# Performance work log

Hardware: AMD Instinct MI355X
Metric: run time of the kernel (lower is better)

## Reference

```python
import jax, jax.numpy as jnp
import numpy as np

B, S, E, H = 4, 4096, 1024, 16
D = E // H          # head dim 64
C = 128             # chunk_size
O = 32              # overlap_size
KCTX = C + O        # context length for chunks > 0
SCALE = 1.0 / np.sqrt(D)


def setup_inputs() -> dict:
    key = jax.random.key(0)
    ks = jax.random.split(key, 11)
    s = 1.0 / np.sqrt(E)
    f32 = jnp.float32
    return {
        "query": jax.random.normal(ks[0], (B, S, E), f32),
        "key_in": jax.random.normal(ks[1], (B, S, E), f32),
        "value": jax.random.normal(ks[2], (B, S, E), f32),
        "Wq": jax.random.normal(ks[3], (E, E), f32) * s,
        "bq": jnp.zeros((E,), f32),
        "Wk": jax.random.normal(ks[4], (E, E), f32) * s,
        "bk": jnp.zeros((E,), f32),
        "Wv": jax.random.normal(ks[5], (E, E), f32) * s,
        "bv": jnp.zeros((E,), f32),
        "Wo": jax.random.normal(ks[6], (E, E), f32) * s,
        "bo": jnp.zeros((E,), f32),
    }


def _attn(q, k, v):
    # q: [..., Lq, H, D], k/v: [..., Lk, H, D] -> [..., Lq, E]
    scores = jnp.einsum("...qhd,...khd->...hqk", q, k) * SCALE
    p = jax.nn.softmax(scores, axis=-1)
    o = jnp.einsum("...hqk,...khd->...qhd", p, v)
    return o.reshape(o.shape[:-2] + (E,))


def reference(query, key_in, value, Wq, bq, Wk, bk, Wv, bv, Wo, bo):
    # position-wise projections (done once; identical to per-chunk projection)
    q = (query @ Wq + bq).reshape(B, S, H, D)
    k = (key_in @ Wk + bk).reshape(B, S, H, D)
    v = (value @ Wv + bv).reshape(B, S, H, D)

    n = S // C  # number of chunks

    # chunk 0: self-attention over first C positions, all C outputs kept
    out0 = _attn(q[:, :C], k[:, :C], v[:, :C])  # [B, C, E]

    # chunks 1..n-1: torch code drops the first O query outputs of each chunk,
    # so only queries at positions i*C+O .. (i+1)*C-1 survive. Each softmax row
    # depends only on its own query, so compute just the kept rows.
    qr = q[:, C:].reshape(B, n - 1, C, H, D)[:, :, O:]  # [B, n-1, C-O, H, D]
    # overlapping kv context windows: [i*C - O, (i+1)*C) of length C+O
    idx = jnp.arange(1, n)[:, None] * C - O + jnp.arange(KCTX)[None, :]  # [n-1, KCTX]
    kr = k[:, idx]  # [B, n-1, KCTX, H, D]
    vr = v[:, idx]
    outr = _attn(qr, kr, vr)               # [B, n-1, C-O, E]
    outr = outr.reshape(B, (n - 1) * (C - O), E)

    out = jnp.concatenate([out0, outr], axis=1)  # [B, C + (n-1)*(C-O), E]
    return out @ Wo + bo
```

## Files before the change

kernel.cpp:

```cpp
#include <hip/hip_runtime.h>
#include <hip/hip_bf16.h>

typedef __bf16 bf16x8 __attribute__((ext_vector_type(8)));
typedef float f32x4 __attribute__((ext_vector_type(4)));
typedef unsigned short u16;
typedef unsigned int u32;

#define DEV __device__ __forceinline__
#define MFMA16 __builtin_amdgcn_mfma_f32_16x16x32_bf16

DEV u16 f2b(float f) {
  __hip_bfloat16 h = __float2bfloat16(f);
  return __builtin_bit_cast(u16, h);
}

DEV void gl_lds16(const u16* g, u16* l) {
  __builtin_amdgcn_global_load_lds(
      (const __attribute__((address_space(1))) void*)g,
      (__attribute__((address_space(3))) void*)l, 16, 0, 0);
}

__global__ __launch_bounds__(256) void wcvt_all(
    const float* __restrict__ Wq, const float* __restrict__ Wk,
    const float* __restrict__ Wv, const float* __restrict__ Wo,
    u16* __restrict__ WtQ, u16* __restrict__ WtK,
    u16* __restrict__ WtV, u16* __restrict__ WtO,
    const float* __restrict__ query, u16* __restrict__ qc,
    const float* __restrict__ key_in, u16* __restrict__ kc,
    const float* __restrict__ value, u16* __restrict__ vc) {
  __shared__ u16 ls[64 * 80];
  const int t = threadIdx.x;
  const int bid = blockIdx.x;
  if (bid < 1024) {
    const int wsel = bid >> 8;
    const float* W = (wsel == 0) ? Wq : (wsel == 1) ? Wk : (wsel == 2) ? Wv : Wo;
    u16* Wt = (wsel == 0) ? WtQ : (wsel == 1) ? WtK : (wsel == 2) ? WtV : WtO;
    const int tb = bid & 255;
    const int bn = (tb & 15) << 6;
    const int bk = (tb >> 4) << 6;
#pragma unroll
    for (int rr = 0; rr < 4; ++rr) {
      const int r = (t >> 4) + (rr << 4);
      const int cc = (t & 15) << 2;
      const float4 v = *reinterpret_cast<const float4*>(&W[(size_t)(bk + r) * 1024 + bn + cc]);
      ls[(cc + 0) * 80 + r] = f2b(v.x);
      ls[(cc + 1) * 80 + r] = f2b(v.y);
      ls[(cc + 2) * 80 + r] = f2b(v.z);
      ls[(cc + 3) * 80 + r] = f2b(v.w);
    }
    __syncthreads();
#pragma unroll
    for (int it = 0; it < 2; ++it) {
      const int idx = t + (it << 8);
      const int n = idx >> 3, c8 = idx & 7;
      const uint4 o = *reinterpret_cast<const uint4*>(&ls[n * 80 + (c8 << 3)]);
      *reinterpret_cast<uint4*>(&Wt[(size_t)(bn + n) * 1024 + bk + (c8 << 3)]) = o;
    }
  }
  const int nthr = (int)gridDim.x * 256;
#pragma unroll
  for (int s = 0; s < 3; ++s) {
    const float* src = (s == 0) ? query : (s == 1) ? key_in : value;
    u16* dst = (s == 0) ? qc : (s == 1) ? kc : vc;
#pragma unroll
    for (int it = 0; it < 4; ++it) {
      const size_t i = (size_t)it * nthr + bid * 256 + t;
      const float4 a = *reinterpret_cast<const float4*>(src + i * 8);
      const float4 b = *reinterpret_cast<const float4*>(src + i * 8 + 4);
      union { u16 sx[8]; uint4 u; } o;
      o.sx[0] = f2b(a.x); o.sx[1] = f2b(a.y); o.sx[2] = f2b(a.z); o.sx[3] = f2b(a.w);
      o.sx[4] = f2b(b.x); o.sx[5] = f2b(b.y); o.sx[6] = f2b(b.z); o.sx[7] = f2b(b.w);
      *reinterpret_cast<uint4*>(dst + i * 8) = o.u;
    }
  }
}

#define MF_CL(PR, PC, AF, BF)                                                  \
  asm volatile("s_waitcnt lgkmcnt(0)" ::: "memory");                           \
  __builtin_amdgcn_sched_barrier(0);                                           \
  __builtin_amdgcn_s_setprio(1);                                               \
  _Pragma("unroll") for (int i = 0; i < 4; ++i)                                \
  _Pragma("unroll") for (int j = 0; j < 2; ++j) {                              \
    acc[(PR)*4 + i][(PC)*2 + j] =                                              \
        MFMA16(AF[i][0], BF[j][0], acc[(PR)*4 + i][(PC)*2 + j], 0, 0, 0);      \
    acc[(PR)*4 + i][(PC)*2 + j] =                                              \
        MFMA16(AF[i][1], BF[j][1], acc[(PR)*4 + i][(PC)*2 + j], 0, 0, 0);      \
  }                                                                            \
  __builtin_amdgcn_s_setprio(0);

#define BAR()  __builtin_amdgcn_s_barrier()
#define SBAR() __builtin_amdgcn_sched_barrier(0)

template <int OUT_F32>
__global__ __launch_bounds__(512, 2) void gemm256(
    const u16* __restrict__ A, const u16* __restrict__ Bt,
    const float* __restrict__ bias, void* __restrict__ Cp,
    const int M, const int N, const int K) {
  __shared__ u16 smem[65536];
  u16* const AbA[2] = {smem, smem + 16384};
  u16* const BbA[2] = {smem + 32768, smem + 49152};
  const int NT = K >> 6;
  const int tid = threadIdx.x;
  const int lane = tid & 63;
  const int w = tid >> 6;
  const int c = lane & 15, g = lane >> 4;

  const int nwg = (int)gridDim.x;
  const int q = nwg >> 3, r = nwg & 7;
  const int xcd = (int)blockIdx.x & 7, loc = (int)blockIdx.x >> 3;
  const int bid = (xcd < r ? xcd * (q + 1) : r * (q + 1) + (xcd - r) * q) + loc;
  const int ntN = N >> 8;
  const int bm = bid / ntN, bn = bid - bm * ntN;
  const int m0 = bm << 8, n0 = bn << 8;

  const int rl = lane >> 3;
  const int swc = ((lane & 7) ^ rl) << 3;
  const int wrow = w << 3;
  const int wm = (w >> 2) << 7, wn = (w & 3) << 6;

  auto stA64 = [&](int t, int row0) {
    u16* b = AbA[t & 1];
    gl_lds16(A + (size_t)(m0 + row0 + wrow + rl) * K + (t << 6) + swc,
             &b[(row0 + wrow) << 6]);
  };
  auto stB32 = [&](int t, int ra, int rb) {
    u16* b = BbA[t & 1];
    const int r0 = (w < 4) ? (ra + (w << 3)) : (rb + ((w - 4) << 3));
    gl_lds16(Bt + (size_t)(n0 + r0 + rl) * K + (t << 6) + swc, &b[r0 << 6]);
  };

  const int sK0 = (g ^ (c & 7)) << 3;
  const int sK1 = ((4 + g) ^ (c & 7)) << 3;
  auto rdA = [&](u16* Ac, int poff, bf16x8 (&dst)[4][2]) {
#pragma unroll
    for (int mi = 0; mi < 4; ++mi) {
      const int ro = (wm + poff + (mi << 4) + c) << 6;
      dst[mi][0] = *reinterpret_cast<const bf16x8*>(&Ac[ro + sK0]);
      dst[mi][1] = *reinterpret_cast<const bf16x8*>(&Ac[ro + sK1]);
    }
  };
  auto rdB = [&](u16* Bc, int poff, bf16x8 (&dst)[2][2]) {
#pragma unroll
    for (int ni = 0; ni < 2; ++ni) {
      const int ro = (wn + poff + (ni << 4) + c) << 6;
      dst[ni][0] = *reinterpret_cast<const bf16x8*>(&Bc[ro + sK0]);
      dst[ni][1] = *reinterpret_cast<const bf16x8*>(&Bc[ro + sK1]);
    }
  };

  f32x4 acc[8][4];
#pragma unroll
  for (int mi = 0; mi < 8; ++mi)
#pragma unroll
    for (int ni = 0; ni < 4; ++ni) acc[mi][ni] = f32x4{0.f, 0.f, 0.f, 0.f};

  stA64(0, 0); stA64(0, 128); stB32(0, 0, 64); stB32(0, 128, 192);
  stA64(0, 64); stA64(0, 192); stB32(0, 32, 96); stB32(0, 160, 224);
  if (NT > 1) { stA64(1, 0); stA64(1, 128); stB32(1, 0, 64); stB32(1, 128, 192); }
  SBAR();
  asm volatile("s_waitcnt vmcnt(4)" ::: "memory");
  SBAR(); BAR();

  bf16x8 af[4][2], b0f[2][2], b1f[2][2];
  for (int t2 = 0; t2 < NT; t2 += 2) {
#pragma unroll
    for (int half = 0; half < 2; ++half) {
      const int t = t2 + half;
      u16* const Ac = AbA[half];
      u16* const Bc = BbA[half];
      const int tn = t + 1, tn2 = t + 2;
      rdA(Ac, 0, af);
      rdB(Bc, 0, b0f);
      if (tn < NT) { stA64(tn, 64); stA64(tn, 192); }
      BAR();
      MF_CL(0, 0, af, b0f);
      BAR(); SBAR();
      rdB(Bc, 32, b1f);
      if (tn < NT) { stB32(tn, 32, 96); stB32(tn, 160, 224); }
      BAR();
      MF_CL(0, 1, af, b1f);
      BAR(); SBAR();
      rdA(Ac, 64, af);
      if (tn2 < NT) { stA64(tn2, 0); stA64(tn2, 128); }
      BAR();
      MF_CL(1, 0, af, b0f);
      BAR(); SBAR();
      if (tn2 < NT) { stB32(tn2, 0, 64); stB32(tn2, 128, 192); }
      BAR();
      MF_CL(1, 1, af, b1f);
      if (tn2 < NT) {
        asm volatile("s_waitcnt vmcnt(4)" ::: "memory");
      } else {
        asm volatile("s_waitcnt vmcnt(0)" ::: "memory");
      }
      SBAR();
      BAR(); SBAR();
    }
  }

  float bv[4];
#pragma unroll
  for (int ni = 0; ni < 4; ++ni) bv[ni] = bias[n0 + wn + (ni << 4) + c];

  if (!OUT_F32) {
    u16* Cb = (u16*)Cp;
#pragma unroll
    for (int mi = 0; mi < 8; ++mi)
#pragma unroll
      for (int ni = 0; ni < 4; ++ni)
#pragma unroll
        for (int rr = 0; rr < 4; ++rr)
          smem[(wm + (mi << 4) + (g << 2) + rr) * 256 + wn + (ni << 4) + c] =
              f2b(acc[mi][ni][rr] + bv[ni]);
    __syncthreads();
#pragma unroll
    for (int i = 0; i < 16; ++i) {
      const int idx = (i << 9) + tid;
      const int row = idx >> 5, sl = idx & 31;
      if (m0 + row < M)
        *reinterpret_cast<uint4*>(&Cb[(size_t)(m0 + row) * N + n0 + (sl << 3)]) =
            *reinterpret_cast<const uint4*>(&smem[row * 256 + (sl << 3)]);
    }
  } else {
    float* Cf = (float*)Cp;
    float* fs = (float*)smem;
#pragma unroll
    for (int hh = 0; hh < 2; ++hh) {
      __syncthreads();
      if ((w >> 2) == hh) {
#pragma unroll
        for (int mi = 0; mi < 8; ++mi)
#pragma unroll
          for (int ni = 0; ni < 4; ++ni)
#pragma unroll
            for (int rr = 0; rr < 4; ++rr)
              fs[((mi << 4) + (g << 2) + rr) * 256 + wn + (ni << 4) + c] =
                  acc[mi][ni][rr] + bv[ni];
      }
      __syncthreads();
#pragma unroll
      for (int i = 0; i < 16; ++i) {
        const int idx = (i << 9) + tid;
        const int row = idx >> 6, sl = idx & 63;
        if (m0 + (hh << 7) + row < M)
          *reinterpret_cast<float4*>(&Cf[(size_t)(m0 + (hh << 7) + row) * N + n0 + (sl << 2)]) =
              *reinterpret_cast<const float4*>(&fs[row * 256 + (sl << 2)]);
      }
    }
  }
}

#define VT_STR 200
#define PS_STR 168

template <int NKT>
DEV void attn_process(const u16* __restrict__ Qg, const u16* __restrict__ Kg,
                      u16* __restrict__ Og, const u16* Vt, u16* Pw,
                      int b, int h, int qpos0, int kpos0, int obase, int nqt,
                      int wv, int lane) {
  const int c = lane & 15, g = lane >> 4;
  constexpr float SC = 0.18033688f;
  for (int qt = wv; qt < nqt; qt += 2) {
    bf16x8 aq[2];
#pragma unroll
    for (int kk = 0; kk < 2; ++kk)
      aq[kk] = *reinterpret_cast<const bf16x8*>(
          Qg + ((size_t)(b * 4096 + qpos0 + (qt << 4) + c)) * 1024 + h * 64 + (kk << 5) + (g << 3));

    f32x4 sacc[NKT];
#pragma unroll
    for (int i = 0; i < NKT; ++i) sacc[i] = f32x4{0.f, 0.f, 0.f, 0.f};
#pragma unroll
    for (int kt = 0; kt < NKT; ++kt) {
#pragma unroll
      for (int kk = 0; kk < 2; ++kk) {
        const bf16x8 bk = *reinterpret_cast<const bf16x8*>(
            Kg + ((size_t)(b * 4096 + kpos0 + (kt << 4) + c)) * 1024 + h * 64 + (kk << 5) + (g << 3));
        sacc[kt] = MFMA16(bk, aq[kk], sacc[kt], 0, 0, 0);
      }
    }

    float mx = -3.0e38f;
#pragma unroll
    for (int kt = 0; kt < NKT; ++kt)
#pragma unroll
      for (int rr = 0; rr < 4; ++rr) mx = fmaxf(mx, sacc[kt][rr]);
    mx = fmaxf(mx, __shfl_xor(mx, 16, 64));
    mx = fmaxf(mx, __shfl_xor(mx, 32, 64));
    mx *= SC;
    float sum = 0.f;
#pragma unroll
    for (int kt = 0; kt < NKT; ++kt) {
      u16 e[4];
#pragma unroll
      for (int rr = 0; rr < 4; ++rr) {
        const float p = exp2f(sacc[kt][rr] * SC - mx);
        sum += p;
        e[rr] = f2b(p);
      }
      uint2 pk;
      pk.x = (u32)e[0] | ((u32)e[1] << 16);
      pk.y = (u32)e[2] | ((u32)e[3] << 16);
      *reinterpret_cast<uint2*>(&Pw[c * PS_STR + (kt << 4) + (g << 2)]) = pk;
    }
    sum += __shfl_xor(sum, 16, 64);
    sum += __shfl_xor(sum, 32, 64);
    const float rs = 1.f / sum;

    asm volatile("s_waitcnt lgkmcnt(0)" ::: "memory");
    __builtin_amdgcn_sched_barrier(0);

    f32x4 oacc[4];
#pragma unroll
    for (int nd = 0; nd < 4; ++nd) oacc[nd] = f32x4{0.f, 0.f, 0.f, 0.f};
#pragma unroll
    for (int u = 0; u < NKT / 2; ++u) {
      const bf16x8 pa = *reinterpret_cast<const bf16x8*>(&Pw[c * PS_STR + (u << 5) + (g << 3)]);
#pragma unroll
      for (int nd = 0; nd < 4; ++nd) {
        const int d = (nd << 4) + c;
        const int a = (u << 2) + g;
        const int us = (a & 24) | ((a ^ (d >> 3)) & 7);
        const bf16x8 vbf = *reinterpret_cast<const bf16x8*>(&Vt[d * VT_STR + (us << 3)]);
        oacc[nd] = MFMA16(vbf, pa, oacc[nd], 0, 0, 0);
      }
    }

    const size_t orow = (size_t)(b * 3104 + obase + (qt << 4) + c);
#pragma unroll
    for (int nd = 0; nd < 4; ++nd) {
      u16 e[4];
#pragma unroll
      for (int rr = 0; rr < 4; ++rr) e[rr] = f2b(oacc[nd][rr] * rs);
      uint2 ov;
      ov.x = (u32)e[0] | ((u32)e[1] << 16);
      ov.y = (u32)e[2] | ((u32)e[3] << 16);
      *reinterpret_cast<uint2*>(&Og[orow * 1024 + h * 64 + (nd << 4) + (g << 2)]) = ov;
    }
  }
}

__global__ __launch_bounds__(128) void attn_kernel(
    const u16* __restrict__ Qg, const u16* __restrict__ Kg,
    const u16* __restrict__ Vg, u16* __restrict__ Og) {
  __shared__ u16 Vt[64 * VT_STR];
  __shared__ u16 Ps[2 * 16 * PS_STR];
  const int bid = blockIdx.x;
  const int b = bid >> 9;
  const int ch = (bid >> 4) & 31;
  const int h = bid & 15;
  const int t = threadIdx.x, wv = t >> 6, lane = t & 63;
  int qpos0, kpos0, obase, nk;
  if (ch == 0) { qpos0 = 0; kpos0 = 0; obase = 0; nk = 128; }
  else { qpos0 = (ch << 7) + 32; kpos0 = (ch << 7) - 32; obase = 128 + (ch - 1) * 96; nk = 160; }

  const size_t vbase = ((size_t)(b * 4096 + kpos0)) * 1024 + h * 64;
  const int c8 = t & 7, rg = t >> 3;
#pragma unroll
  for (int p = 0; p < 3; ++p) {
    const int k0 = (rg << 2) + (p << 6);
    if (k0 < nk) {
      u32 w[4][4];
#pragma unroll
      for (int rr = 0; rr < 4; ++rr) {
        const uint4 v = *reinterpret_cast<const uint4*>(Vg + vbase + (size_t)(k0 + rr) * 1024 + (c8 << 3));
        w[rr][0] = v.x; w[rr][1] = v.y; w[rr][2] = v.z; w[rr][3] = v.w;
      }
      const int k8 = k0 >> 3;
      const int us = (k8 & 24) | ((k8 ^ c8) & 7);
      const int base = (us << 3) + (k0 & 7);
#pragma unroll
      for (int dw = 0; dw < 4; ++dw) {
        uint2 lo, hi;
        lo.x = __builtin_amdgcn_perm(w[1][dw], w[0][dw], 0x05040100u);
        lo.y = __builtin_amdgcn_perm(w[3][dw], w[2][dw], 0x05040100u);
        hi.x = __builtin_amdgcn_perm(w[1][dw], w[0][dw], 0x07060302u);
        hi.y = __builtin_amdgcn_perm(w[3][dw], w[2][dw], 0x07060302u);
        const int d0 = (c8 << 3) + (dw << 1);
        *reinterpret_cast<uint2*>(&Vt[d0 * VT_STR + base]) = lo;
        *reinterpret_cast<uint2*>(&Vt[(d0 + 1) * VT_STR + base]) = hi;
      }
    }
  }
  __syncthreads();

  u16* Pw = Ps + wv * (16 * PS_STR);
  if (ch == 0)
    attn_process<8>(Qg, Kg, Og, Vt, Pw, b, h, qpos0, kpos0, obase, 8, wv, lane);
  else
    attn_process<10>(Qg, Kg, Og, Vt, Pw, b, h, qpos0, kpos0, obase, 6, wv, lane);
}

extern "C" void kernel_launch(void* const* d_in, const int* in_sizes, int n_in,
                              void* d_out, int out_size, void* d_ws, size_t ws_size,
                              hipStream_t stream) {
  (void)in_sizes; (void)n_in; (void)out_size;
  const float* query  = (const float*)d_in[0];
  const float* key_in = (const float*)d_in[1];
  const float* value  = (const float*)d_in[2];
  const float* Wq = (const float*)d_in[3];
  const float* bq = (const float*)d_in[4];
  const float* Wk = (const float*)d_in[5];
  const float* bk = (const float*)d_in[6];
  const float* Wv = (const float*)d_in[7];
  const float* bv = (const float*)d_in[8];
  const float* Wo = (const float*)d_in[9];
  const float* bo = (const float*)d_in[10];

  char* ws = (char*)d_ws;
  const size_t WSZ = 2097152;
  const size_t ASZ = 33554432;
  u16* WtQ = (u16*)(ws + 0 * WSZ);
  u16* WtK = (u16*)(ws + 1 * WSZ);
  u16* WtV = (u16*)(ws + 2 * WSZ);
  u16* WtO = (u16*)(ws + 3 * WSZ);
  u16* s0  = (u16*)(ws + 4 * WSZ);
  u16* qb  = (u16*)(ws + 4 * WSZ + 1 * ASZ);
  u16* kb  = (u16*)(ws + 4 * WSZ + 2 * ASZ);
  u16* s3  = (u16*)(ws + 4 * WSZ + 3 * ASZ);
  if (ws_size < (size_t)142606336) return;

  u16* qc = s0;
  u16* kc = s3;
  u16* vc = (u16*)d_out;
  u16* vb = s3;
  u16* ao = s0;

  wcvt_all<<<2048, 256, 0, stream>>>(Wq, Wk, Wv, Wo, WtQ, WtK, WtV, WtO,
                                     query, qc, key_in, kc, value, vc);

  gemm256<0><<<256, 512, 0, stream>>>(qc, WtQ, bq, qb, 16384, 1024, 1024);
  gemm256<0><<<256, 512, 0, stream>>>(kc, WtK, bk, kb, 16384, 1024, 1024);
  gemm256<0><<<256, 512, 0, stream>>>(vc, WtV, bv, vb, 16384, 1024, 1024);

  attn_kernel<<<2048, 128, 0, stream>>>(qb, kb, vb, ao);

  gemm256<1><<<196, 512, 0, stream>>>(ao, WtO, bo, (float*)d_out, 12416, 1024, 1024);
}
```

Baseline: 241.0 us.

## Overlap key/value fp32-to-bf16 conversion with preceding projection GEMMs

The standalone pre-conversion kernel now converts only the weights and the query activations. The key and value conversions move into two extra waves added to the Q and K projection GEMM blocks (640 threads instead of 512). Those waves stream fp32 to bf16 in lockstep with the GEMM waves' barriers, so memory-bound conversion runs alongside compute-bound MFMA work. The cost is fewer registers per thread under the larger launch bound, and a barrier count that must exactly match the GEMM main loop.

```diff
diff --git a/kernel.cpp b/kernel.cpp
--- a/kernel.cpp
+++ b/kernel.cpp
@@ -13,6 +13,7 @@
   __hip_bfloat16 h = __float2bfloat16(f);
   return __builtin_bit_cast(u16, h);
 }
+DEV u32 pk2(float x, float y) { return (u32)f2b(x) | ((u32)f2b(y) << 16); }
 
 DEV void gl_lds16(const u16* g, u16* l) {
   __builtin_amdgcn_global_load_lds(
@@ -20,14 +21,12 @@
       (__attribute__((address_space(3))) void*)l, 16, 0, 0);
 }
 
-__global__ __launch_bounds__(256) void wcvt_all(
+__global__ __launch_bounds__(256) void precvt(
     const float* __restrict__ Wq, const float* __restrict__ Wk,
     const float* __restrict__ Wv, const float* __restrict__ Wo,
     u16* __restrict__ WtQ, u16* __restrict__ WtK,
     u16* __restrict__ WtV, u16* __restrict__ WtO,
-    const float* __restrict__ query, u16* __restrict__ qc,
-    const float* __restrict__ key_in, u16* __restrict__ kc,
-    const float* __restrict__ value, u16* __restrict__ vc) {
+    const float4* __restrict__ query, uint4* __restrict__ qc) {
   __shared__ u16 ls[64 * 80];
   const int t = threadIdx.x;
   const int bid = blockIdx.x;
@@ -56,22 +55,26 @@
       const uint4 o = *reinterpret_cast<const uint4*>(&ls[n * 80 + (c8 << 3)]);
       *reinterpret_cast<uint4*>(&Wt[(size_t)(bn + n) * 1024 + bk + (c8 << 3)]) = o;
     }
-  }
-  const int nthr = (int)gridDim.x * 256;
-#pragma unroll
-  for (int s = 0; s < 3; ++s) {
-    const float* src = (s == 0) ? query : (s == 1) ? key_in : value;
-    u16* dst = (s == 0) ? qc : (s == 1) ? kc : vc;
-#pragma unroll
-    for (int it = 0; it < 4; ++it) {
-      const size_t i = (size_t)it * nthr + bid * 256 + t;
-      const float4 a = *reinterpret_cast<const float4*>(src + i * 8);
-      const float4 b = *reinterpret_cast<const float4*>(src + i * 8 + 4);
-      union { u16 sx[8]; uint4 u; } o;
-      o.sx[0] = f2b(a.x); o.sx[1] = f2b(a.y); o.sx[2] = f2b(a.z); o.sx[3] = f2b(a.w);
-      o.sx[4] = f2b(b.x); o.sx[5] = f2b(b.y); o.sx[6] = f2b(b.z); o.sx[7] = f2b(b.w);
-      *reinterpret_cast<uint4*>(dst + i * 8) = o.u;
-    }
+    return;
+  }
+  const int blk = bid - 1024;
+  float4 a[8];
+#pragma unroll
+  for (int j = 0; j < 4; ++j) {
+    const size_t ci = (size_t)blk * 1024 + j * 256 + t;
+    a[2 * j]     = query[2 * ci];
+    a[2 * j + 1] = query[2 * ci + 1];
+  }
+  asm volatile("" ::: "memory");
+#pragma unroll
+  for (int j = 0; j < 4; ++j) {
+    const size_t ci = (size_t)blk * 1024 + j * 256 + t;
+    uint4 o;
+    o.x = pk2(a[2 * j].x, a[2 * j].y);
+    o.y = pk2(a[2 * j].z, a[2 * j].w);
+    o.z = pk2(a[2 * j + 1].x, a[2 * j + 1].y);
+    o.w = pk2(a[2 * j + 1].z, a[2 * j + 1].w);
+    qc[ci] = o;
   }
 }
 
@@ -91,10 +94,11 @@
 #define BAR()  __builtin_amdgcn_s_barrier()
 #define SBAR() __builtin_amdgcn_sched_barrier(0)
 
-template <int OUT_F32>
-__global__ __launch_bounds__(512, 2) void gemm256(
+template <int DO_CVT, int OUT_F32>
+__global__ __launch_bounds__(DO_CVT ? 640 : 512, 2) void gemm256(
     const u16* __restrict__ A, const u16* __restrict__ Bt,
     const float* __restrict__ bias, void* __restrict__ Cp,
+    const float4* __restrict__ csrc, uint2* __restrict__ cdst,
     const int M, const int N, const int K) {
   __shared__ u16 smem[65536];
   u16* const AbA[2] = {smem, smem + 16384};
@@ -104,6 +108,37 @@
   const int lane = tid & 63;
   const int w = tid >> 6;
   const int c = lane & 15, g = lane >> 4;
+
+  if (DO_CVT && w >= 8) {
+    const int l = tid - 512;
+    const size_t b4 = (size_t)blockIdx.x * 16384 + l;
+    float4 Ax = csrc[b4 + 0];
+    float4 Bx = csrc[b4 + 128];
+    float4 Cx = csrc[b4 + 256];
+    float4 Dx = csrc[b4 + 384];
+    BAR();
+    for (int s = 0; s < 128; s += 4) {
+      uint2 o;
+      o.x = pk2(Ax.x, Ax.y); o.y = pk2(Ax.z, Ax.w);
+      cdst[b4 + (size_t)s * 128] = o;
+      if (s < 124) Ax = csrc[b4 + (size_t)(s + 4) * 128];
+      BAR();
+      o.x = pk2(Bx.x, Bx.y); o.y = pk2(Bx.z, Bx.w);
+      cdst[b4 + (size_t)(s + 1) * 128] = o;
+      if (s < 124) Bx = csrc[b4 + (size_t)(s + 5) * 128];
+      BAR();
+      o.x = pk2(Cx.x, Cx.y); o.y = pk2(Cx.z, Cx.w);
+      cdst[b4 + (size_t)(s + 2) * 128] = o;
+      if (s < 124) Cx = csrc[b4 + (size_t)(s + 6) * 128];
+      BAR();
+      o.x = pk2(Dx.x, Dx.y); o.y = pk2(Dx.z, Dx.w);
+      cdst[b4 + (size_t)(s + 3) * 128] = o;
+      if (s < 124) Dx = csrc[b4 + (size_t)(s + 7) * 128];
+      BAR();
+    }
+    BAR();
+    return;
+  }
 
   const int nwg = (int)gridDim.x;
   const int q = nwg >> 3, r = nwg & 7;
@@ -426,14 +461,20 @@
   u16* vb = s3;
   u16* ao = s0;
 
-  wcvt_all<<<2048, 256, 0, stream>>>(Wq, Wk, Wv, Wo, WtQ, WtK, WtV, WtO,
-                                     query, qc, key_in, kc, value, vc);
-
-  gemm256<0><<<256, 512, 0, stream>>>(qc, WtQ, bq, qb, 16384, 1024, 1024);
-  gemm256<0><<<256, 512, 0, stream>>>(kc, WtK, bk, kb, 16384, 1024, 1024);
-  gemm256<0><<<256, 512, 0, stream>>>(vc, WtV, bv, vb, 16384, 1024, 1024);
+  precvt<<<3072, 256, 0, stream>>>(Wq, Wk, Wv, Wo, WtQ, WtK, WtV, WtO,
+                                   (const float4*)query, (uint4*)qc);
+
+  gemm256<1, 0><<<256, 640, 0, stream>>>(qc, WtQ, bq, qb,
+                                         (const float4*)key_in, (uint2*)kc,
+                                         16384, 1024, 1024);
+  gemm256<1, 0><<<256, 640, 0, stream>>>(kc, WtK, bk, kb,
+                                         (const float4*)value, (uint2*)vc,
+                                         16384, 1024, 1024);
+  gemm256<0, 0><<<256, 512, 0, stream>>>(vc, WtV, bv, vb,
+                                         nullptr, nullptr, 16384, 1024, 1024);
 
   attn_kernel<<<2048, 128, 0, stream>>>(qb, kb, vb, ao);
 
-  gemm256<1><<<196, 512, 0, stream>>>(ao, WtO, bo, (float*)d_out, 12416, 1024, 1024);
-}
+  gemm256<0, 1><<<196, 512, 0, stream>>>(ao, WtO, bo, (float*)d_out,
+                                         nullptr, nullptr, 12416, 1024, 1024);
+}
```

Result: slower. 659.3 us (+173.6%).
